# Kernel tuning notes

Hardware: AMD Instinct MI355X
Metric: run time of the kernel (lower is better)

## Reference

```python
import jax, jax.numpy as jnp
import numpy as np

DIM = 1028


def setup_inputs() -> dict:
    key = jax.random.key(0)
    ks = jax.random.split(key, 11)
    B, N = 8, 2048
    s = 0.02
    x = jax.random.normal(ks[0], (B, N, DIM), dtype=jnp.float32)
    Wq = jax.random.normal(ks[1], (DIM, DIM), dtype=jnp.float32) * s
    bq = jax.random.normal(ks[2], (DIM,), dtype=jnp.float32) * s
    Wk = jax.random.normal(ks[3], (DIM, DIM), dtype=jnp.float32) * s
    bk = jax.random.normal(ks[4], (DIM,), dtype=jnp.float32) * s
    Wv = jax.random.normal(ks[5], (DIM, DIM), dtype=jnp.float32) * s
    bv = jax.random.normal(ks[6], (DIM,), dtype=jnp.float32) * s
    We = jax.random.normal(ks[7], (4 * DIM, DIM), dtype=jnp.float32) * s
    be = jax.random.normal(ks[8], (4 * DIM,), dtype=jnp.float32) * s
    Wo = jax.random.normal(ks[9], (DIM, 4 * DIM), dtype=jnp.float32) * s
    bo = jax.random.normal(ks[10], (DIM,), dtype=jnp.float32) * s
    return {"x": x, "Wq": Wq, "bq": bq, "Wk": Wk, "bk": bk, "Wv": Wv,
            "bv": bv, "We": We, "be": be, "Wo": Wo, "bo": bo}


def reference(x, Wq, bq, Wk, bk, Wv, bv, We, be, Wo, bo):
    # x: [B, N, D]. torch Linear weight is [out, in] -> x @ W.T + b
    q = jnp.einsum('bnd,ed->bne', x, Wq) + bq
    k = jnp.einsum('bnd,ed->bne', x, Wk) + bk
    v = jnp.einsum('bnd,ed->bne', x, Wv) + bv
    scores = jnp.einsum('bqd,bkd->bqk', q, k) / jnp.sqrt(jnp.float32(DIM))
    w = jax.nn.softmax(scores, axis=-1)          # [B, N, N]
    attn = jnp.einsum('bqk,bkd->bqd', w, v)      # [B, N, D]
    h = jax.nn.gelu(jnp.einsum('bnd,hd->bnh', attn, We) + be, approximate=False)
    out = jnp.einsum('bnh,dh->bnd', h, Wo) + bo
    return out + x
```

## Files before the change

kernel.cpp:

```cpp
#include <hip/hip_runtime.h>
#include <hip/hip_bf16.h>
#include <cstdint>
#include <cmath>


typedef __bf16 bf16;
typedef __bf16 bf16x8 __attribute__((ext_vector_type(8)));
typedef float  f32x4  __attribute__((ext_vector_type(4)));

#define D_REAL   1028
#define D_PADK   1088
#define D_PADN   1152
#define H_REAL   4112
#define H_PAD    4224
#define NTOK     2048
#define NB       8
#define MTOT     (NB*NTOK)
#define SLAB_X   ((size_t)NTOK*D_PADK)
#define SLAB_S   ((size_t)NTOK*NTOK)
#define WSLAB    ((size_t)D_PADN*D_PADK)
#define VSLAB    ((size_t)D_PADN*NTOK)

__device__ __forceinline__ void async16(const void* g, void* l) {
    __builtin_amdgcn_global_load_lds(
        (__attribute__((address_space(1))) void*)(uintptr_t)g,
        (__attribute__((address_space(3))) void*)(uint32_t)(uintptr_t)l,
        16, 0, 0);
}

#define MFMA_(a, b, c) __builtin_amdgcn_mfma_f32_16x16x32_bf16(a, b, c, 0, 0, 0)

template <int EPI, bool XPIN>
__global__ __launch_bounds__(512, 2)
void gemm256(const bf16* __restrict__ A, size_t strideA,
             const bf16* __restrict__ B, size_t strideB,
             const float* __restrict__ bias, size_t strideBias,
             void* __restrict__ Out, size_t strideOut,
             bf16* __restrict__ OutV,
             int K, int outPitch, int colBound, float scale,
             const float* __restrict__ resid)
{
    __shared__ __attribute__((aligned(16))) bf16 sAB[4][256 * 64];

    int bx, by, bz;
    if (XPIN) {
        bz = blockIdx.x; by = blockIdx.y; bx = blockIdx.z;
    } else {
        const int nx   = gridDim.x;
        const int nwg  = nx * gridDim.y;
        const int orig = blockIdx.y * nx + blockIdx.x;
        const int q    = nwg >> 3;
        const int wg   = (orig & 7) * q + (orig >> 3);
        bx = wg % nx; by = wg / nx; bz = blockIdx.z;
    }

    A += (size_t)bz * strideA;
    B += (size_t)bz * strideB;
    if (bias) bias += (size_t)bz * strideBias;

    const int tid  = threadIdx.x;
    const int lane = tid & 63;
    const int wv   = tid >> 6;
    const int wm   = wv >> 2;
    const int wn   = wv & 3;

    const int    NT  = K >> 6;
    const size_t K64 = (size_t)K * 64;

    const int sRow = tid >> 3;
    const int sCh  = (tid & 7) ^ (sRow & 7);
    const bf16* gA = A + (size_t)(by * 256 + sRow) * K + sCh * 8;
    const bf16* gB = B + (size_t)(bx * 256 + sRow) * K + sCh * 8;
    const int ldsOff = sRow * 64 + (tid & 7) * 8;

#define STAGE_A(tt) do {                                           \
        const bf16* g_ = gA + (size_t)(tt) * 64;                   \
        bf16* l_ = &sAB[(tt) & 1][0] + ldsOff;                     \
        async16(g_,           l_);                                 \
        async16(g_ +     K64, l_ +  4096);                         \
        async16(g_ + 2 * K64, l_ +  8192);                         \
        async16(g_ + 3 * K64, l_ + 12288);                         \
    } while (0)
#define STAGE_B_HALF(tt, h) do {                                   \
        const bf16* g_ = gB + (size_t)(tt) * 64 + (2 * (h)) * K64; \
        bf16* l_ = &sAB[2 + ((tt) & 1)][0] + ldsOff + (2*(h))*4096;\
        async16(g_,       l_);                                     \
        async16(g_ + K64, l_ + 4096);                              \
    } while (0)

    const int lr   = lane & 15;
    const int lq   = lane >> 4;
    const int rsw  = lr & 7;
    const int aRow = (wm * 128 + lr) * 64;
    const int bRow = (wn * 64  + lr) * 64;
    const int sl0  = (lq ^ rsw) << 3;
    const int sl1  = ((lq + 4) ^ rsw) << 3;

#define LDA_(i, s) (*(const bf16x8*)&sAc[aRow + (i) * 1024 + (s)])
#define LDB_(j, s) (*(const bf16x8*)&sBc[bRow + (j) * 1024 + (s)])

    f32x4 acc[8][4] = {};

#define MM(i, a0, a1) do {                                  \
        acc[i][0] = MFMA_(a0, bfr[0][0], acc[i][0]);        \
        acc[i][0] = MFMA_(a1, bfr[0][1], acc[i][0]);        \
        acc[i][1] = MFMA_(a0, bfr[1][0], acc[i][1]);        \
        acc[i][1] = MFMA_(a1, bfr[1][1], acc[i][1]);        \
        acc[i][2] = MFMA_(a0, bfr[2][0], acc[i][2]);        \
        acc[i][2] = MFMA_(a1, bfr[2][1], acc[i][2]);        \
        acc[i][3] = MFMA_(a0, bfr[3][0], acc[i][3]);        \
        acc[i][3] = MFMA_(a1, bfr[3][1], acc[i][3]);        \
    } while (0)

#define PH_ENTER() do {                                          \
        __builtin_amdgcn_s_barrier();                            \
        asm volatile("s_waitcnt lgkmcnt(0)" ::: "memory");       \
        __builtin_amdgcn_sched_barrier(0);                       \
        __builtin_amdgcn_s_setprio(1);                           \
    } while (0)
#define PH_EXIT() do {                                           \
        __builtin_amdgcn_s_setprio(0);                           \
        __builtin_amdgcn_s_barrier();                            \
    } while (0)

    STAGE_A(0); STAGE_B_HALF(0, 0); STAGE_B_HALF(0, 1);
    STAGE_A(1); STAGE_B_HALF(1, 0); STAGE_B_HALF(1, 1);
    asm volatile("s_waitcnt vmcnt(8)" ::: "memory");
    __builtin_amdgcn_s_barrier();

    for (int t = 0; t < NT; ++t) {
        const int bcur = t & 1;
        const bf16* sAc = sAB[bcur];
        const bf16* sBc = sAB[2 + bcur];
        bf16x8 bfr[4][2];
        bf16x8 aA, aB, aC, aD;

        bfr[0][0] = LDB_(0, sl0); bfr[0][1] = LDB_(0, sl1);
        bfr[1][0] = LDB_(1, sl0); bfr[1][1] = LDB_(1, sl1);
        bfr[2][0] = LDB_(2, sl0); bfr[2][1] = LDB_(2, sl1);
        bfr[3][0] = LDB_(3, sl0); bfr[3][1] = LDB_(3, sl1);
        aA = LDA_(0, sl0); aB = LDA_(0, sl1);
        aC = LDA_(1, sl0); aD = LDA_(1, sl1);
        if (t >= 1 && t + 1 < NT) STAGE_A(t + 1);
        PH_ENTER();
        MM(0, aA, aB); MM(1, aC, aD);
        PH_EXIT();

        aA = LDA_(2, sl0); aB = LDA_(2, sl1);
        aC = LDA_(3, sl0); aD = LDA_(3, sl1);
        if (t + 2 < NT) STAGE_B_HALF(t + 2, 0);
        PH_ENTER();
        MM(2, aA, aB); MM(3, aC, aD);
        PH_EXIT();

        aA = LDA_(4, sl0); aB = LDA_(4, sl1);
        aC = LDA_(5, sl0); aD = LDA_(5, sl1);
        if (t + 2 < NT) STAGE_B_HALF(t + 2, 1);
        PH_ENTER();
        MM(4, aA, aB); MM(5, aC, aD);
        PH_EXIT();

        aA = LDA_(6, sl0); aB = LDA_(6, sl1);
        aC = LDA_(7, sl0); aD = LDA_(7, sl1);
        __builtin_amdgcn_s_barrier();
        asm volatile("s_waitcnt lgkmcnt(0)" ::: "memory");
        __builtin_amdgcn_sched_barrier(0);
        __builtin_amdgcn_s_setprio(1);
        MM(6, aA, aB); MM(7, aC, aD);
        __builtin_amdgcn_s_setprio(0);
        if (t + 2 < NT)       asm volatile("s_waitcnt vmcnt(4)" ::: "memory");
        else if (t + 2 == NT) asm volatile("s_waitcnt vmcnt(0)" ::: "memory");
        __builtin_amdgcn_s_barrier();
        __builtin_amdgcn_sched_barrier(0);
    }

    #pragma unroll
    for (int i = 0; i < 8; ++i) {
        const int rowBase = by * 256 + wm * 128 + i * 16 + lq * 4;
        #pragma unroll
        for (int j = 0; j < 4; ++j) {
            f32x4 v = acc[i][j];
            const int cg = bx * 256 + wn * 64 + j * 16 + lr;
            if (cg >= colBound) continue;
            const float bs = bias ? bias[cg] : 0.0f;
            #pragma unroll
            for (int r = 0; r < 4; ++r) {
                const int mg = rowBase + r;
                const float val = v[r];
                if (EPI == 0) {
                    ((bf16*)Out + (size_t)bz * strideOut)[(size_t)mg * outPitch + cg] =
                        (bf16)(val + bs);
                } else if (EPI == 3) {
                    const float u = val + bs;
                    const float g = 0.5f * u * (1.0f + erff(u * 0.70710678118654752f));
                    ((bf16*)Out)[(size_t)mg * outPitch + cg] = (bf16)g;
                } else if (EPI == 4) {
                    ((float*)Out)[(size_t)mg * outPitch + cg] =
                        val + bs + resid[(size_t)mg * outPitch + cg];
                } else if (EPI == 5) {
                    const int grp = cg / D_PADN;
                    const int c   = cg - grp * D_PADN;
                    const float u = val + bs;
                    if (grp < 2) {
                        if (c < D_PADK)
                            ((bf16*)Out)[(size_t)bz * 2 * SLAB_X + (size_t)grp * SLAB_X +
                                         (size_t)mg * D_PADK + c] = (bf16)u;
                    } else {
                        OutV[(size_t)bz * VSLAB + (size_t)c * NTOK + mg] = (bf16)u;
                    }
                } else {
                    ((bf16*)Out + (size_t)bz * strideOut)[(size_t)mg * outPitch + cg] =
                        (bf16)(val * scale);
                }
            }
        }
    }
#undef STAGE_A
#undef STAGE_B_HALF
#undef LDA_
#undef LDB_
#undef MM
#undef PH_ENTER
#undef PH_EXIT
}

__global__ __launch_bounds__(256)
void cvt_pad(const float* __restrict__ src, int R, int C,
             bf16* __restrict__ dst, int CP)
{
    const int c = blockIdx.x * 256 + threadIdx.x;
    const int r = blockIdx.y;
    if (c >= CP) return;
    const float v = (r < R && c < C) ? src[(size_t)r * C + c] : 0.0f;
    dst[(size_t)r * CP + c] = (bf16)v;
}

__global__ __launch_bounds__(256)
void pad_bias(const float* __restrict__ src, int n, float* __restrict__ dst, int np)
{
    const int i = blockIdx.x * 256 + threadIdx.x;
    if (i < np) dst[i] = (i < n) ? src[i] : 0.0f;
}

__global__ __launch_bounds__(256)
void softmax_ip(bf16* __restrict__ S)
{
    const int row  = blockIdx.x * 4 + (threadIdx.x >> 6);
    const int lane = threadIdx.x & 63;
    bf16* s = S + (size_t)row * NTOK + lane * 8;

    float v[32];
    #pragma unroll
    for (int j = 0; j < 4; ++j) {
        bf16x8 t = *(const bf16x8*)(s + j * 512);
        #pragma unroll
        for (int e = 0; e < 8; ++e) v[j * 8 + e] = (float)t[e];
    }
    float m = -1e30f;
    #pragma unroll
    for (int i = 0; i < 32; ++i) m = fmaxf(m, v[i]);
    #pragma unroll
    for (int off = 32; off > 0; off >>= 1) m = fmaxf(m, __shfl_xor(m, off, 64));

    float sum = 0.0f;
    #pragma unroll
    for (int i = 0; i < 32; ++i) { v[i] = __expf(v[i] - m); sum += v[i]; }
    #pragma unroll
    for (int off = 32; off > 0; off >>= 1) sum += __shfl_xor(sum, off, 64);
    const float inv = 1.0f / sum;

    #pragma unroll
    for (int j = 0; j < 4; ++j) {
        bf16x8 t;
        #pragma unroll
        for (int e = 0; e < 8; ++e) t[e] = (bf16)(v[j * 8 + e] * inv);
        *(bf16x8*)(s + j * 512) = t;
    }
}

#define OFF_WQKV   0u
#define OFF_WE     7520256u
#define OFF_WO     16711680u
#define OFF_BQKV   26443776u
#define OFF_BE     26457600u
#define OFF_XBF    26474496u
#define OFF_VT     62126080u
#define OFF_SCR    99874816u
#define QS_BYTES   8912896u
#define SS_BYTES   8388608u

extern "C" void kernel_launch(void* const* d_in, const int* in_sizes, int n_in,
                              void* d_out, int out_size, void* d_ws, size_t ws_size,
                              hipStream_t stream)
{
    const float* x  = (const float*)d_in[0];
    const float* Wq = (const float*)d_in[1];
    const float* bq = (const float*)d_in[2];
    const float* Wk = (const float*)d_in[3];
    const float* bk = (const float*)d_in[4];
    const float* Wv = (const float*)d_in[5];
    const float* bv = (const float*)d_in[6];
    const float* We = (const float*)d_in[7];
    const float* be = (const float*)d_in[8];
    const float* Wo = (const float*)d_in[9];
    const float* bo = (const float*)d_in[10];

    char* ws = (char*)d_ws;
    bf16*  Wqkv = (bf16*)(ws + OFF_WQKV);
    bf16*  WeP  = (bf16*)(ws + OFF_WE);
    bf16*  WoP  = (bf16*)(ws + OFF_WO);
    float* Bqkv = (float*)(ws + OFF_BQKV);
    float* BeP  = (float*)(ws + OFF_BE);
    bf16*  Xbf  = (bf16*)(ws + OFF_XBF);
    bf16*  Vt   = (bf16*)(ws + OFF_VT);
    char*  scr  = ws + OFF_SCR;

    const size_t avail = ws_size > OFF_SCR ? ws_size - OFF_SCR : 0;
    const size_t perG  = (size_t)QS_BYTES + SS_BYTES;
    int G = (avail >= 8 * perG) ? 8 : (avail >= 4 * perG) ? 4
          : (avail >= 2 * perG) ? 2 : 1;
    int R = (avail >= 69206016u) ? 8192 : (avail >= 34603008u) ? 4096 : 2048;

    bf16* Qs = (bf16*)scr;
    bf16* Ss = (bf16*)(scr + (size_t)G * QS_BYTES);
    bf16* Hb = (bf16*)scr;

    const dim3 blk(256);
    const dim3 blkG(512);
    const float inv_sqrt_d = (float)(1.0 / sqrt((double)D_REAL));

    cvt_pad<<<dim3(5, MTOT), blk, 0, stream>>>(x, MTOT, D_REAL, Xbf, D_PADK);
    cvt_pad<<<dim3(5, D_PADN), blk, 0, stream>>>(Wq, D_REAL, D_REAL, Wqkv, D_PADK);
    cvt_pad<<<dim3(5, D_PADN), blk, 0, stream>>>(Wk, D_REAL, D_REAL, Wqkv + WSLAB, D_PADK);
    cvt_pad<<<dim3(5, D_PADN), blk, 0, stream>>>(Wv, D_REAL, D_REAL, Wqkv + 2 * WSLAB, D_PADK);
    cvt_pad<<<dim3(5, H_PAD), blk, 0, stream>>>(We, H_REAL, D_REAL, WeP, D_PADK);
    cvt_pad<<<dim3(17, D_PADN), blk, 0, stream>>>(Wo, D_REAL, H_REAL, WoP, H_PAD);
    pad_bias<<<dim3(5), blk, 0, stream>>>(bq, D_REAL, Bqkv, D_PADN);
    pad_bias<<<dim3(5), blk, 0, stream>>>(bk, D_REAL, Bqkv + D_PADN, D_PADN);
    pad_bias<<<dim3(5), blk, 0, stream>>>(bv, D_REAL, Bqkv + 2 * D_PADN, D_PADN);
    pad_bias<<<dim3(17), blk, 0, stream>>>(be, H_REAL, BeP, H_PAD);

    for (int g0 = 0; g0 < NB; g0 += G) {
        gemm256<5, false><<<dim3(14, 8, G), blkG, 0, stream>>>(
            Xbf + (size_t)g0 * SLAB_X, SLAB_X, Wqkv, 0, Bqkv, 0,
            Qs, 0, Vt + (size_t)g0 * VSLAB,
            D_PADK, 0, 3456, 1.0f, nullptr);
        gemm256<6, true><<<dim3(G, 8, 8), blkG, 0, stream>>>(
            Qs, 2 * SLAB_X, Qs + SLAB_X, 2 * SLAB_X, nullptr, 0,
            Ss, SLAB_S, nullptr, D_PADK, NTOK, NTOK, inv_sqrt_d, nullptr);
        softmax_ip<<<dim3(G * 512), blk, 0, stream>>>(Ss);
        gemm256<0, true><<<dim3(G, 8, 5), blkG, 0, stream>>>(
            Ss, SLAB_S, Vt + (size_t)g0 * VSLAB, VSLAB, nullptr, 0,
            Xbf + (size_t)g0 * SLAB_X, SLAB_X, nullptr,
            NTOK, D_PADK, D_PADK, 1.0f, nullptr);
    }

    for (int r0 = 0; r0 < MTOT; r0 += R) {
        gemm256<3, false><<<dim3(17, R / 256, 1), blkG, 0, stream>>>(
            Xbf + (size_t)r0 * D_PADK, 0, WeP, 0, BeP, 0,
            Hb, 0, nullptr, D_PADK, H_PAD, H_PAD, 1.0f, nullptr);
        gemm256<4, false><<<dim3(5, R / 256, 1), blkG, 0, stream>>>(
            Hb, 0, WoP, 0, bo, 0,
            (float*)d_out + (size_t)r0 * D_REAL, 0, nullptr,
            H_PAD, D_REAL, D_REAL, 1.0f, x + (size_t)r0 * D_REAL);
    }
}
```

Before: 1.149 ms.

## Replace phased ping-pong GEMM schedule with simple double-buffered loop

Removes the four-phase schedule, which used priority bumps, per-phase barriers and staggered half-B prefetch two tiles ahead. In its place is a straightforward loop: issue the loads for tile t+1, wait for tile t, then run all 64 MFMAs with the LDS reads interleaved. This cuts barrier count and scheduling constraints. The cost is a shallower prefetch distance and less explicit overlap of memory with compute.

Measured after the change: 1.136 ms. About the same (-1.1%).

```diff
diff --git a/kernel.cpp b/kernel.cpp
--- a/kernel.cpp
+++ b/kernel.cpp
@@ -81,11 +81,13 @@
         async16(g_ + 2 * K64, l_ +  8192);                         \
         async16(g_ + 3 * K64, l_ + 12288);                         \
     } while (0)
-#define STAGE_B_HALF(tt, h) do {                                   \
-        const bf16* g_ = gB + (size_t)(tt) * 64 + (2 * (h)) * K64; \
-        bf16* l_ = &sAB[2 + ((tt) & 1)][0] + ldsOff + (2*(h))*4096;\
-        async16(g_,       l_);                                     \
-        async16(g_ + K64, l_ + 4096);                              \
+#define STAGE_B(tt) do {                                           \
+        const bf16* g_ = gB + (size_t)(tt) * 64;                   \
+        bf16* l_ = &sAB[2 + ((tt) & 1)][0] + ldsOff;               \
+        async16(g_,           l_);                                 \
+        async16(g_ +     K64, l_ +  4096);                         \
+        async16(g_ + 2 * K64, l_ +  8192);                         \
+        async16(g_ + 3 * K64, l_ + 12288);                         \
     } while (0)
 
     const int lr   = lane & 15;
@@ -101,75 +103,43 @@
 
     f32x4 acc[8][4] = {};
 
-#define MM(i, a0, a1) do {                                  \
-        acc[i][0] = MFMA_(a0, bfr[0][0], acc[i][0]);        \
-        acc[i][0] = MFMA_(a1, bfr[0][1], acc[i][0]);        \
-        acc[i][1] = MFMA_(a0, bfr[1][0], acc[i][1]);        \
-        acc[i][1] = MFMA_(a1, bfr[1][1], acc[i][1]);        \
-        acc[i][2] = MFMA_(a0, bfr[2][0], acc[i][2]);        \
-        acc[i][2] = MFMA_(a1, bfr[2][1], acc[i][2]);        \
-        acc[i][3] = MFMA_(a0, bfr[3][0], acc[i][3]);        \
-        acc[i][3] = MFMA_(a1, bfr[3][1], acc[i][3]);        \
-    } while (0)
-
-#define PH_ENTER() do {                                          \
-        __builtin_amdgcn_s_barrier();                            \
-        asm volatile("s_waitcnt lgkmcnt(0)" ::: "memory");       \
-        __builtin_amdgcn_sched_barrier(0);                       \
-        __builtin_amdgcn_s_setprio(1);                           \
-    } while (0)
-#define PH_EXIT() do {                                           \
-        __builtin_amdgcn_s_setprio(0);                           \
-        __builtin_amdgcn_s_barrier();                            \
-    } while (0)
-
-    STAGE_A(0); STAGE_B_HALF(0, 0); STAGE_B_HALF(0, 1);
-    STAGE_A(1); STAGE_B_HALF(1, 0); STAGE_B_HALF(1, 1);
-    asm volatile("s_waitcnt vmcnt(8)" ::: "memory");
-    __builtin_amdgcn_s_barrier();
+    STAGE_A(0); STAGE_B(0);
 
     for (int t = 0; t < NT; ++t) {
-        const int bcur = t & 1;
-        const bf16* sAc = sAB[bcur];
-        const bf16* sBc = sAB[2 + bcur];
+        if (t + 1 < NT) {
+            STAGE_A(t + 1);
+            STAGE_B(t + 1);
+            asm volatile("s_waitcnt vmcnt(8)" ::: "memory");
+        } else {
+            asm volatile("s_waitcnt vmcnt(0)" ::: "memory");
+        }
+        __builtin_amdgcn_s_barrier();
+        __builtin_amdgcn_sched_barrier(0);
+
+        const bf16* sAc = &sAB[t & 1][0];
+        const bf16* sBc = &sAB[2 + (t & 1)][0];
+
         bf16x8 bfr[4][2];
-        bf16x8 aA, aB, aC, aD;
-
         bfr[0][0] = LDB_(0, sl0); bfr[0][1] = LDB_(0, sl1);
         bfr[1][0] = LDB_(1, sl0); bfr[1][1] = LDB_(1, sl1);
         bfr[2][0] = LDB_(2, sl0); bfr[2][1] = LDB_(2, sl1);
         bfr[3][0] = LDB_(3, sl0); bfr[3][1] = LDB_(3, sl1);
-        aA = LDA_(0, sl0); aB = LDA_(0, sl1);
-        aC = LDA_(1, sl0); aD = LDA_(1, sl1);
-        if (t >= 1 && t + 1 < NT) STAGE_A(t + 1);
-        PH_ENTER();
-        MM(0, aA, aB); MM(1, aC, aD);
-        PH_EXIT();
-
-        aA = LDA_(2, sl0); aB = LDA_(2, sl1);
-        aC = LDA_(3, sl0); aD = LDA_(3, sl1);
-        if (t + 2 < NT) STAGE_B_HALF(t + 2, 0);
-        PH_ENTER();
-        MM(2, aA, aB); MM(3, aC, aD);
-        PH_EXIT();
-
-        aA = LDA_(4, sl0); aB = LDA_(4, sl1);
-        aC = LDA_(5, sl0); aD = LDA_(5, sl1);
-        if (t + 2 < NT) STAGE_B_HALF(t + 2, 1);
-        PH_ENTER();
-        MM(4, aA, aB); MM(5, aC, aD);
-        PH_EXIT();
-
-        aA = LDA_(6, sl0); aB = LDA_(6, sl1);
-        aC = LDA_(7, sl0); aD = LDA_(7, sl1);
-        __builtin_amdgcn_s_barrier();
+
+        #pragma unroll
+        for (int i = 0; i < 8; ++i) {
+            const bf16x8 a0 = LDA_(i, sl0);
+            const bf16x8 a1 = LDA_(i, sl1);
+            acc[i][0] = MFMA_(a0, bfr[0][0], acc[i][0]);
+            acc[i][1] = MFMA_(a0, bfr[1][0], acc[i][1]);
+            acc[i][2] = MFMA_(a0, bfr[2][0], acc[i][2]);
+            acc[i][3] = MFMA_(a0, bfr[3][0], acc[i][3]);
+            acc[i][0] = MFMA_(a1, bfr[0][1], acc[i][0]);
+            acc[i][1] = MFMA_(a1, bfr[1][1], acc[i][1]);
+            acc[i][2] = MFMA_(a1, bfr[2][1], acc[i][2]);
+            acc[i][3] = MFMA_(a1, bfr[3][1], acc[i][3]);
+        }
+
         asm volatile("s_waitcnt lgkmcnt(0)" ::: "memory");
-        __builtin_amdgcn_sched_barrier(0);
-        __builtin_amdgcn_s_setprio(1);
-        MM(6, aA, aB); MM(7, aC, aD);
-        __builtin_amdgcn_s_setprio(0);
-        if (t + 2 < NT)       asm volatile("s_waitcnt vmcnt(4)" ::: "memory");
-        else if (t + 2 == NT) asm volatile("s_waitcnt vmcnt(0)" ::: "memory");
         __builtin_amdgcn_s_barrier();
         __builtin_amdgcn_sched_barrier(0);
     }
@@ -216,12 +186,9 @@
         }
     }
 #undef STAGE_A
-#undef STAGE_B_HALF
+#undef STAGE_B
 #undef LDA_
 #undef LDB_
-#undef MM
-#undef PH_ENTER
-#undef PH_EXIT
 }
 
 __global__ __launch_bounds__(256)
```
